# Performance work log

Hardware: AMD Instinct MI355X
Metric: run time of the kernel (lower is better)

The kernel has to match this reference:

```python
import jax, jax.numpy as jnp
import numpy as np

TOKENS, D_MODEL, D_FF = 8192, 2048, 8192


def _ternary_quant(w):
    # TernaryQuantizer.forward: scale = mean(|w|); round(clamp(w/scale, -1, 1)) * scale
    # (torch casts to int8 then multiplies by float scale -> same float values)
    scale = jnp.mean(jnp.abs(w))
    return jnp.round(jnp.clip(w / scale, -1.0, 1.0)) * scale


def _quantize_activations(x):
    # scale = 127 / max(|x|); round(clamp(x*scale, -127, 127)) / scale
    scale = 127.0 / jnp.max(jnp.abs(x))
    return jnp.round(jnp.clip(x * scale, -127.0, 127.0)) / scale


def setup_inputs() -> dict:
    key = jax.random.key(0)
    k1, k2, k3, k4, k5 = jax.random.split(key, 5)
    x = jax.random.normal(k1, (TOKENS, D_MODEL), dtype=jnp.float32)
    # torch Linear init scale (kaiming-uniform-ish); keep values modest
    W1 = jax.random.normal(k2, (D_FF, D_MODEL), dtype=jnp.float32) * (1.0 / np.sqrt(D_MODEL))
    b1 = jax.random.normal(k3, (D_FF,), dtype=jnp.float32) * 0.01
    W2 = jax.random.normal(k4, (D_MODEL, D_FF), dtype=jnp.float32) * (1.0 / np.sqrt(D_FF))
    b2 = jax.random.normal(k5, (D_MODEL,), dtype=jnp.float32) * 0.01
    return {"x": x, "W1": W1, "b1": b1, "W2": W2, "b2": b2}


def reference(x, W1, b1, W2, b2):
    # BitNetModel.forward over [BitLinear, GELU, BitLinear]:
    # quantize_activations before each BitLinear; BitLinear uses ternary weights.
    h = _quantize_activations(x) @ _ternary_quant(W1).T + b1  # [TOKENS, D_FF]
    h = jax.nn.gelu(h, approximate=False)  # torch nn.GELU default = exact erf
    out = _quantize_activations(h) @ _ternary_quant(W2).T + b2  # [TOKENS, D_MODEL]
    return out
```

## Files before the change

### kernel.cpp

```cpp
#include <hip/hip_runtime.h>
#include <hip/hip_bf16.h>
#include <math.h>


#define TOKENS 8192
#define DMODEL 2048
#define DFF    8192
#define NW     16777216

using i32x4 = __attribute__((ext_vector_type(4))) int;

#define GLD16_TO_LDS(g, l) __builtin_amdgcn_global_load_lds( \
    (const __attribute__((address_space(1))) void*)(g), \
    (__attribute__((address_space(3))) void*)(l), 16, 0, 0)

__global__ void reduce_abs_kernel(const float* __restrict__ in, int n,
                                  float* __restrict__ sum_out,
                                  unsigned int* __restrict__ max_out) {
    int idx = blockIdx.x * blockDim.x + threadIdx.x;
    int stride = gridDim.x * blockDim.x;
    const float4* in4 = (const float4*)in;
    int n4 = n >> 2;
    float s = 0.f, m = 0.f;
    for (int i = idx; i < n4; i += stride) {
        float4 v = in4[i];
        float ax = fabsf(v.x), ay = fabsf(v.y), az = fabsf(v.z), aw = fabsf(v.w);
        s += ax + ay + az + aw;
        m = fmaxf(m, fmaxf(fmaxf(ax, ay), fmaxf(az, aw)));
    }
    #pragma unroll
    for (int off = 32; off; off >>= 1) {
        s += __shfl_xor(s, off);
        m = fmaxf(m, __shfl_xor(m, off));
    }
    __shared__ float ss[4], sm[4];
    int wave = threadIdx.x >> 6, lane = threadIdx.x & 63;
    if (lane == 0) { ss[wave] = s; sm[wave] = m; }
    __syncthreads();
    if (threadIdx.x == 0) {
        float ts = ss[0] + ss[1] + ss[2] + ss[3];
        float tm = fmaxf(fmaxf(sm[0], sm[1]), fmaxf(sm[2], sm[3]));
        atomicAdd(sum_out, ts);
        atomicMax(max_out, __float_as_uint(tm));
    }
}

__global__ void quant_act_kernel(const float* __restrict__ in,
                                 signed char* __restrict__ out, int n,
                                 const unsigned int* __restrict__ maxp) {
    float scale = 127.0f / __uint_as_float(*maxp);
    int idx = blockIdx.x * blockDim.x + threadIdx.x;
    int stride = gridDim.x * blockDim.x;
    const float4* in4 = (const float4*)in;
    unsigned int* out4 = (unsigned int*)out;
    int n4 = n >> 2;
    for (int i = idx; i < n4; i += stride) {
        float4 v = in4[i];
        int q0 = (int)rintf(fminf(fmaxf(v.x * scale, -127.f), 127.f));
        int q1 = (int)rintf(fminf(fmaxf(v.y * scale, -127.f), 127.f));
        int q2 = (int)rintf(fminf(fmaxf(v.z * scale, -127.f), 127.f));
        int q3 = (int)rintf(fminf(fmaxf(v.w * scale, -127.f), 127.f));
        out4[i] = (q0 & 0xff) | ((q1 & 0xff) << 8) | ((q2 & 0xff) << 16) | ((q3 & 0xff) << 24);
    }
}

__global__ void quant_w_kernel(const float* __restrict__ in,
                               signed char* __restrict__ out, int n,
                               const float* __restrict__ sump) {
    float s = *sump / 16777216.0f;
    int idx = blockIdx.x * blockDim.x + threadIdx.x;
    int stride = gridDim.x * blockDim.x;
    const float4* in4 = (const float4*)in;
    unsigned int* out4 = (unsigned int*)out;
    int n4 = n >> 2;
    for (int i = idx; i < n4; i += stride) {
        float4 v = in4[i];
        int q0 = (int)rintf(fminf(fmaxf(v.x / s, -1.f), 1.f));
        int q1 = (int)rintf(fminf(fmaxf(v.y / s, -1.f), 1.f));
        int q2 = (int)rintf(fminf(fmaxf(v.z / s, -1.f), 1.f));
        int q3 = (int)rintf(fminf(fmaxf(v.w / s, -1.f), 1.f));
        out4[i] = (q0 & 0xff) | ((q1 & 0xff) << 8) | ((q2 & 0xff) << 16) | ((q3 & 0xff) << 24);
    }
}

template <int EPI>
__global__ __launch_bounds__(256) void gemm_i8(
    const signed char* __restrict__ A, const signed char* __restrict__ B,
    void* __restrict__ Cv, const float* __restrict__ bias,
    int K, int N, const float* __restrict__ sc,
    unsigned int* __restrict__ max_out)
{
    __shared__ __align__(16) unsigned char sA[128 * 64];
    __shared__ __align__(16) unsigned char sB[128 * 64];
    __shared__ float smax[4];

    const int tid = threadIdx.x;
    const int lane = tid & 63;
    const int wave = tid >> 6;
    const int wm = wave >> 1;
    const int wn = wave & 1;
    const long rowBase = (long)blockIdx.y * 128;
    const long colBase = (long)blockIdx.x * 128;
    const signed char* Ab = A + rowBase * (long)K;
    const signed char* Bb = B + colBase * (long)K;

    i32x4 acc[4][4] = {};

    const int o0 = tid * 16;

    for (int kk = 0; kk < K; kk += 64) {
        #pragma unroll
        for (int it = 0; it < 2; ++it) {
            int o = it * 4096 + o0;
            int r = o >> 6, cb = o & 63;
            GLD16_TO_LDS(Ab + (long)r * K + kk + cb, &sA[o]);
            GLD16_TO_LDS(Bb + (long)r * K + kk + cb, &sB[o]);
        }
        __syncthreads();

        i32x4 a[4], b[4];
        #pragma unroll
        for (int m = 0; m < 4; ++m) {
            int off = (wm * 64 + m * 16 + (lane & 15)) * 64 + (lane >> 4) * 16;
            a[m] = *(const i32x4*)(&sA[off]);
        }
        #pragma unroll
        for (int n = 0; n < 4; ++n) {
            int off = (wn * 64 + n * 16 + (lane & 15)) * 64 + (lane >> 4) * 16;
            b[n] = *(const i32x4*)(&sB[off]);
        }
        #pragma unroll
        for (int m = 0; m < 4; ++m)
            #pragma unroll
            for (int n = 0; n < 4; ++n)
                acc[m][n] = __builtin_amdgcn_mfma_i32_16x16x64_i8(a[m], b[n], acc[m][n], 0, 0, 0);
        __syncthreads();
    }

    float wmax = 0.f;
    if (EPI == 0 || EPI == 2 || EPI == 3) {
        float scale_w = sc[0] / 16777216.0f;
        float maxx = __uint_as_float(((const unsigned int*)sc)[3]);
        float alpha = scale_w * maxx / 127.0f;
        float qscale = 0.f;
        if (EPI == 3)
            qscale = 127.0f / __uint_as_float(((const unsigned int*)sc)[6]);
        #pragma unroll
        for (int m = 0; m < 4; ++m) {
            int row_l = wm * 64 + m * 16 + ((lane >> 4) * 4);
            #pragma unroll
            for (int n = 0; n < 4; ++n) {
                int col = (int)colBase + wn * 64 + n * 16 + (lane & 15);
                float bv = bias[col];
                #pragma unroll
                for (int r = 0; r < 4; ++r) {
                    long grow = rowBase + row_l + r;
                    float v = (float)acc[m][n][r] * alpha + bv;
                    float g = 0.5f * v * (1.0f + erff(v * 0.70710678118654752f));
                    if (EPI == 0) ((float*)Cv)[grow * N + col] = g;
                    if (EPI == 3) {
                        float q = rintf(fminf(fmaxf(g * qscale, -127.f), 127.f));
                        ((signed char*)Cv)[grow * N + col] = (signed char)(int)q;
                    }
                    wmax = fmaxf(wmax, fabsf(g));
                }
            }
        }
    } else {
        float scale_w = sc[1] / 16777216.0f;
        float maxg = __uint_as_float(((const unsigned int*)sc)[6]);
        float alpha = scale_w * maxg / 127.0f;
        #pragma unroll
        for (int m = 0; m < 4; ++m) {
            int row_l = wm * 64 + m * 16 + ((lane >> 4) * 4);
            #pragma unroll
            for (int n = 0; n < 4; ++n) {
                int col = (int)colBase + wn * 64 + n * 16 + (lane & 15);
                float bv = bias[col];
                #pragma unroll
                for (int r = 0; r < 4; ++r) {
                    long grow = rowBase + row_l + r;
                    ((float*)Cv)[grow * N + col] = (float)acc[m][n][r] * alpha + bv;
                }
            }
        }
    }

    if (EPI == 0 || EPI == 2) {
        #pragma unroll
        for (int off = 32; off; off >>= 1)
            wmax = fmaxf(wmax, __shfl_xor(wmax, off));
        if (lane == 0) smax[wave] = wmax;
        __syncthreads();
        if (tid == 0) {
            float bm = fmaxf(fmaxf(smax[0], smax[1]), fmaxf(smax[2], smax[3]));
            atomicMax(max_out, __float_as_uint(bm));
        }
    }
}

extern "C" void kernel_launch(void* const* d_in, const int* in_sizes, int n_in,
                              void* d_out, int out_size, void* d_ws, size_t ws_size,
                              hipStream_t stream) {
    const float* x  = (const float*)d_in[0];
    const float* W1 = (const float*)d_in[1];
    const float* b1 = (const float*)d_in[2];
    const float* W2 = (const float*)d_in[3];
    const float* b2 = (const float*)d_in[4];
    float* out = (float*)d_out;

    char* ws = (char*)d_ws;
    float* sc = (float*)ws;
    signed char* xq  = (signed char*)(ws + 256);
    signed char* w1q = xq + (size_t)NW;
    signed char* w2q = w1q + (size_t)NW;
    signed char* hq  = w2q + (size_t)NW;
    float* h = (float*)(hq + (size_t)TOKENS * DFF);
    size_t needA = 256 + 3ULL * NW + (size_t)TOKENS * DFF * 5ULL;
    bool bigws = ws_size >= needA;

    hipMemsetAsync(sc, 0, 64, stream);

    reduce_abs_kernel<<<1024, 256, 0, stream>>>(x,  NW, &sc[2], (unsigned int*)&sc[3]);
    reduce_abs_kernel<<<1024, 256, 0, stream>>>(W1, NW, &sc[0], (unsigned int*)&sc[4]);
    reduce_abs_kernel<<<1024, 256, 0, stream>>>(W2, NW, &sc[1], (unsigned int*)&sc[5]);

    quant_act_kernel<<<1024, 256, 0, stream>>>(x, xq, NW, (const unsigned int*)&sc[3]);
    quant_w_kernel<<<1024, 256, 0, stream>>>(W1, w1q, NW, &sc[0]);
    quant_w_kernel<<<1024, 256, 0, stream>>>(W2, w2q, NW, &sc[1]);

    dim3 g1(DFF / 128, TOKENS / 128);
    if (bigws) {
        gemm_i8<0><<<g1, 256, 0, stream>>>(xq, w1q, (void*)h, b1, DMODEL, DFF, sc,
                                           (unsigned int*)&sc[6]);
        quant_act_kernel<<<4096, 256, 0, stream>>>(h, hq, TOKENS * DFF,
                                                   (const unsigned int*)&sc[6]);
    } else {
        gemm_i8<2><<<g1, 256, 0, stream>>>(xq, w1q, nullptr, b1, DMODEL, DFF, sc,
                                           (unsigned int*)&sc[6]);
        gemm_i8<3><<<g1, 256, 0, stream>>>(xq, w1q, (void*)hq, b1, DMODEL, DFF, sc,
                                           (unsigned int*)&sc[6]);
    }

    dim3 g2(DMODEL / 128, TOKENS / 128);
    gemm_i8<1><<<g2, 256, 0, stream>>>(hq, w2q, (void*)out, b2, DFF, DMODEL, sc, nullptr);
}
```

Measured before the change: 1.196 ms.

## Use 256x256 double-buffered int8 GEMM tiles with swizzled block order and fast GELU

Replaces the 128x128 single-buffered int8 MFMA GEMM with a 256x256 tile kernel of 512 threads. It double-buffers LDS with async global-to-LDS loads and uses a pre-fragmented LDS layout so fragments are read as contiguous 16-byte lanes. Block IDs are remapped across 8 groups to improve L2 locality. The exact erff is replaced by an Abramowitz-Stegun polynomial with a fast reciprocal and exp. This aims to raise data reuse and overlap loads with MFMA, at the cost of higher register and LDS pressure and a small GELU approximation error.

New measurement: 997.9 us. 16.6% less time.

```diff
diff --git a/kernel.cpp b/kernel.cpp
--- a/kernel.cpp
+++ b/kernel.cpp
@@ -83,58 +83,94 @@
     }
 }
 
+__device__ __forceinline__ float gelu_exact(float v) {
+    float x  = v * 0.70710678118654752f;
+    float ax = fabsf(x);
+    float t  = __builtin_amdgcn_rcpf(__builtin_fmaf(0.3275911f, ax, 1.0f));
+    float p  = __builtin_fmaf(1.061405429f, t, -1.453152027f);
+    p = __builtin_fmaf(p, t, 1.421413741f);
+    p = __builtin_fmaf(p, t, -0.284496736f);
+    p = __builtin_fmaf(p, t, 0.254829592f);
+    p = p * t;
+    float e = __expf(-ax * ax);
+    float erfabs = __builtin_fmaf(-p, e, 1.0f);
+    float er = copysignf(erfabs, x);
+    return 0.5f * v * (1.0f + er);
+}
+
 template <int EPI>
-__global__ __launch_bounds__(256) void gemm_i8(
+__global__ __launch_bounds__(512, 2) void gemm_i8_v2(
     const signed char* __restrict__ A, const signed char* __restrict__ B,
     void* __restrict__ Cv, const float* __restrict__ bias,
-    int K, int N, const float* __restrict__ sc,
+    int K, int N, int nbx_lg2, const float* __restrict__ sc,
     unsigned int* __restrict__ max_out)
 {
-    __shared__ __align__(16) unsigned char sA[128 * 64];
-    __shared__ __align__(16) unsigned char sB[128 * 64];
-    __shared__ float smax[4];
-
-    const int tid = threadIdx.x;
+    __shared__ __align__(16) unsigned char sA[2][16384];
+    __shared__ __align__(16) unsigned char sB[2][16384];
+    __shared__ float smax[8];
+
+    const int tid  = threadIdx.x;
     const int lane = tid & 63;
     const int wave = tid >> 6;
-    const int wm = wave >> 1;
-    const int wn = wave & 1;
-    const long rowBase = (long)blockIdx.y * 128;
-    const long colBase = (long)blockIdx.x * 128;
+    const int wr   = wave >> 2;
+    const int wn   = wave & 3;
+
+    const int cpx = gridDim.x >> 3;
+    const int bid = blockIdx.x;
+    const int nid = (bid & 7) * cpx + (bid >> 3);
+    const int bx  = nid & ((1 << nbx_lg2) - 1);
+    const int by  = nid >> nbx_lg2;
+
+    const long rowBase = (long)by * 256;
+    const long colBase = (long)bx * 256;
     const signed char* Ab = A + rowBase * (long)K;
     const signed char* Bb = B + colBase * (long)K;
-
-    i32x4 acc[4][4] = {};
-
-    const int o0 = tid * 16;
-
-    for (int kk = 0; kk < K; kk += 64) {
+    const int NT = K >> 6;
+
+    i32x4 acc[8][4] = {};
+
+    auto stage = [&](int t, int bf) {
+        const long kk = (long)t << 6;
         #pragma unroll
         for (int it = 0; it < 2; ++it) {
-            int o = it * 4096 + o0;
-            int r = o >> 6, cb = o & 63;
-            GLD16_TO_LDS(Ab + (long)r * K + kk + cb, &sA[o]);
-            GLD16_TO_LDS(Bb + (long)r * K + kk + cb, &sB[o]);
-        }
-        __syncthreads();
-
-        i32x4 a[4], b[4];
-        #pragma unroll
-        for (int m = 0; m < 4; ++m) {
-            int off = (wm * 64 + m * 16 + (lane & 15)) * 64 + (lane >> 4) * 16;
-            a[m] = *(const i32x4*)(&sA[off]);
-        }
-        #pragma unroll
-        for (int n = 0; n < 4; ++n) {
-            int off = (wn * 64 + n * 16 + (lane & 15)) * 64 + (lane >> 4) * 16;
-            b[n] = *(const i32x4*)(&sB[off]);
-        }
-        #pragma unroll
-        for (int m = 0; m < 4; ++m)
+            int off = it * 8192 + tid * 16;
+            int fr  = off >> 10;
+            int kc  = (off >> 8) & 3;
+            int r   = (off >> 4) & 15;
+            long row = (long)(fr * 16 + r);
+            long src = row * K + kk + kc * 16;
+            GLD16_TO_LDS(Ab + src, &sA[bf][off]);
+            GLD16_TO_LDS(Bb + src, &sB[bf][off]);
+        }
+    };
+
+    stage(0, 0);
+    stage(1, 1);
+    asm volatile("s_waitcnt vmcnt(4)" ::: "memory");
+    __builtin_amdgcn_s_barrier();
+
+    for (int t = 0; t < NT; ++t) {
+        const int c = t & 1;
+        i32x4 bfr[4];
+        #pragma unroll
+        for (int n = 0; n < 4; ++n)
+            bfr[n] = *(const i32x4*)&sB[c][(wn * 4 + n) * 1024 + lane * 16];
+        #pragma unroll
+        for (int m = 0; m < 8; ++m) {
+            i32x4 afr = *(const i32x4*)&sA[c][(wr * 8 + m) * 1024 + lane * 16];
             #pragma unroll
             for (int n = 0; n < 4; ++n)
-                acc[m][n] = __builtin_amdgcn_mfma_i32_16x16x64_i8(a[m], b[n], acc[m][n], 0, 0, 0);
-        __syncthreads();
+                acc[m][n] = __builtin_amdgcn_mfma_i32_16x16x64_i8(afr, bfr[n], acc[m][n], 0, 0, 0);
+        }
+        asm volatile("s_waitcnt lgkmcnt(0)" ::: "memory");
+        __builtin_amdgcn_s_barrier();
+        if (t + 2 < NT) {
+            stage(t + 2, c);
+            asm volatile("s_waitcnt vmcnt(4)" ::: "memory");
+        } else {
+            asm volatile("s_waitcnt vmcnt(0)" ::: "memory");
+        }
+        __builtin_amdgcn_s_barrier();
     }
 
     float wmax = 0.f;
@@ -146,8 +182,8 @@
         if (EPI == 3)
             qscale = 127.0f / __uint_as_float(((const unsigned int*)sc)[6]);
         #pragma unroll
-        for (int m = 0; m < 4; ++m) {
-            int row_l = wm * 64 + m * 16 + ((lane >> 4) * 4);
+        for (int m = 0; m < 8; ++m) {
+            int row_l = wr * 128 + m * 16 + ((lane >> 4) * 4);
             #pragma unroll
             for (int n = 0; n < 4; ++n) {
                 int col = (int)colBase + wn * 64 + n * 16 + (lane & 15);
@@ -156,7 +192,7 @@
                 for (int r = 0; r < 4; ++r) {
                     long grow = rowBase + row_l + r;
                     float v = (float)acc[m][n][r] * alpha + bv;
-                    float g = 0.5f * v * (1.0f + erff(v * 0.70710678118654752f));
+                    float g = gelu_exact(v);
                     if (EPI == 0) ((float*)Cv)[grow * N + col] = g;
                     if (EPI == 3) {
                         float q = rintf(fminf(fmaxf(g * qscale, -127.f), 127.f));
@@ -171,8 +207,8 @@
         float maxg = __uint_as_float(((const unsigned int*)sc)[6]);
         float alpha = scale_w * maxg / 127.0f;
         #pragma unroll
-        for (int m = 0; m < 4; ++m) {
-            int row_l = wm * 64 + m * 16 + ((lane >> 4) * 4);
+        for (int m = 0; m < 8; ++m) {
+            int row_l = wr * 128 + m * 16 + ((lane >> 4) * 4);
             #pragma unroll
             for (int n = 0; n < 4; ++n) {
                 int col = (int)colBase + wn * 64 + n * 16 + (lane & 15);
@@ -193,7 +229,9 @@
         if (lane == 0) smax[wave] = wmax;
         __syncthreads();
         if (tid == 0) {
-            float bm = fmaxf(fmaxf(smax[0], smax[1]), fmaxf(smax[2], smax[3]));
+            float bm = smax[0];
+            #pragma unroll
+            for (int w = 1; w < 8; ++w) bm = fmaxf(bm, smax[w]);
             atomicMax(max_out, __float_as_uint(bm));
         }
     }
@@ -229,19 +267,18 @@
     quant_w_kernel<<<1024, 256, 0, stream>>>(W1, w1q, NW, &sc[0]);
     quant_w_kernel<<<1024, 256, 0, stream>>>(W2, w2q, NW, &sc[1]);
 
-    dim3 g1(DFF / 128, TOKENS / 128);
     if (bigws) {
-        gemm_i8<0><<<g1, 256, 0, stream>>>(xq, w1q, (void*)h, b1, DMODEL, DFF, sc,
-                                           (unsigned int*)&sc[6]);
+        gemm_i8_v2<0><<<1024, 512, 0, stream>>>(xq, w1q, (void*)h, b1, DMODEL, DFF, 5,
+                                                sc, (unsigned int*)&sc[6]);
         quant_act_kernel<<<4096, 256, 0, stream>>>(h, hq, TOKENS * DFF,
                                                    (const unsigned int*)&sc[6]);
     } else {
-        gemm_i8<2><<<g1, 256, 0, stream>>>(xq, w1q, nullptr, b1, DMODEL, DFF, sc,
-                                           (unsigned int*)&sc[6]);
-        gemm_i8<3><<<g1, 256, 0, stream>>>(xq, w1q, (void*)hq, b1, DMODEL, DFF, sc,
-                                           (unsigned int*)&sc[6]);
-    }
-
-    dim3 g2(DMODEL / 128, TOKENS / 128);
-    gemm_i8<1><<<g2, 256, 0, stream>>>(hq, w2q, (void*)out, b2, DFF, DMODEL, sc, nullptr);
-}
+        gemm_i8_v2<2><<<1024, 512, 0, stream>>>(xq, w1q, nullptr, b1, DMODEL, DFF, 5,
+                                                sc, (unsigned int*)&sc[6]);
+        gemm_i8_v2<3><<<1024, 512, 0, stream>>>(xq, w1q, (void*)hq, b1, DMODEL, DFF, 5,
+                                                sc, (unsigned int*)&sc[6]);
+    }
+
+    gemm_i8_v2<1><<<256, 512, 0, stream>>>(hq, w2q, (void*)out, b2, DFF, DMODEL, 3,
+                                           sc, nullptr);
+}
```
